# Kernel tuning notes

Hardware: AMD Instinct MI355X
Metric: run time of the kernel (lower is better)

## Reference

```python
import jax, jax.numpy as jnp
import numpy as np

M, K, N = 8192, 4096, 11008  # tokens, in_features, out_features


def setup_inputs() -> dict:
    key = jax.random.key(0)
    k_x, k_w, k_dq, k_is, k_qb = jax.random.split(key, 5)
    x = jax.random.normal(k_x, (M, K), dtype=jnp.float16)
    # int8 per-channel weights, values in [-127, 127]
    weight = jax.random.randint(k_w, (N, K), -127, 128, dtype=jnp.int32).astype(jnp.int8)
    # per-channel dequant scale ~ input_scale * weight_scale (small positive fp32)
    deq_scale = (jax.random.uniform(k_dq, (N,), dtype=jnp.float32) * 0.5 + 0.5) * 1e-4
    # per-tensor input scale (fp16 in the original buffer; kept fp32 here for math)
    input_scale = jax.random.uniform(k_is, (1,), dtype=jnp.float32) * 0.02 + 0.02
    quant_bias = jax.random.randint(k_qb, (N,), -100, 100, dtype=jnp.int32)
    input_offset = jnp.zeros((1,), dtype=jnp.int8)
    return {
        "x": x,
        "weight": weight,
        "deq_scale": deq_scale,
        "input_scale": input_scale,
        "quant_bias": quant_bias,
        "input_offset": input_offset,
    }


def reference(x, weight, deq_scale, input_scale, quant_bias, input_offset):
    # 1) static per-tensor activation quantization: fp16 -> int8
    inv_scale = 1.0 / input_scale.astype(jnp.float32)  # [1]
    xq = jnp.clip(
        jnp.round(x.astype(jnp.float32) * inv_scale) + input_offset.astype(jnp.float32),
        -128.0, 127.0,
    ).astype(jnp.int8)  # [M, K]
    acc = jnp.matmul(xq, weight.T, preferred_element_type=jnp.int32)  # [M, N] int32
    # 3) fused int32 bias add
    acc = acc + quant_bias[None, :]
    # 4) per-channel dequantization -> fp16 output
    out = (acc.astype(jnp.float32) * deq_scale[None, :]).astype(jnp.float16)
    return out
```

## Files before the change

kernel.cpp:

```cpp
#include <hip/hip_runtime.h>


#define MDIM 8192
#define KDIM 4096
#define NDIM 11008

#define BM 128
#define BN 128
#define BK 64
#define TM (MDIM / BM)
#define TN (NDIM / BN)
#define NWG (TM * TN)
#define CPX (NWG / 8)
#define KSTEPS (KDIM / BK)

using int32x4  = __attribute__((ext_vector_type(4))) int;
using int32x16 = __attribute__((ext_vector_type(16))) int;
using floatx4  = __attribute__((ext_vector_type(4))) float;
using uint32x2 = __attribute__((ext_vector_type(2))) unsigned int;

__device__ __forceinline__ void gload_lds16(const void* g, void* l) {
    __builtin_amdgcn_global_load_lds(
        (__attribute__((address_space(1))) unsigned int*)g,
        (__attribute__((address_space(3))) unsigned int*)l,
        16, 0, 0);
}

__device__ __forceinline__ int quant1(float f, float inv, float off) {
    float r = rintf(f * inv) + off;
    r = fminf(127.f, fmaxf(-128.f, r));
    return (int)r;
}

__device__ __forceinline__ int pack4i(int a, int b, int c, int d) {
    return (a & 255) | ((b & 255) << 8) | ((c & 255) << 16) | ((d & 255) << 24);
}

struct Resolved { const float* dq; const int* qb; };
__device__ __forceinline__ Resolved resolve4(const void* p11a, const void* p11b) {
    Resolved r;
    int a_is_dq = 1;
#pragma unroll
    for (int j = 0; j < 8; ++j) {
        const float v = ((const float*)p11a)[j];
        a_is_dq &= (v > 1e-6f) & (v < 1e-2f);
    }
    r.dq = a_is_dq ? (const float*)p11a : (const float*)p11b;
    r.qb = a_is_dq ? (const int*)p11b : (const int*)p11a;
    return r;
}

__device__ __forceinline__ void resolve_scale(const void* p1a, const void* p1b,
                                              float* inv, float* off) {
    const float fa = ((const float*)p1a)[0];
    const int a_is_isc = (fa > 1e-3f) & (fa < 1.0f);
    const float iscv = a_is_isc ? ((const float*)p1a)[0] : ((const float*)p1b)[0];
    *inv = 1.0f / iscv;
    *off = (float)(a_is_isc ? ((const int*)p1b)[0] : ((const int*)p1a)[0]);
}

__global__ __launch_bounds__(256)
void quant_x(const float* __restrict__ X, const void* p1a, const void* p1b,
             signed char* __restrict__ xq) {
    float inv, off;
    resolve_scale(p1a, p1b, &inv, &off);
    const long long nch = (long long)MDIM * KDIM / 8;
    const long long stride = (long long)gridDim.x * 256;
    for (long long i = (long long)blockIdx.x * 256 + threadIdx.x; i < nch; i += stride) {
        floatx4 v0 = ((const floatx4*)X)[2 * i];
        floatx4 v1 = ((const floatx4*)X)[2 * i + 1];
        int q[8];
#pragma unroll
        for (int j = 0; j < 4; ++j) {
            q[j]     = quant1(v0[j], inv, off);
            q[4 + j] = quant1(v1[j], inv, off);
        }
        uint32x2 o;
        o[0] = (unsigned)pack4i(q[0], q[1], q[2], q[3]);
        o[1] = (unsigned)pack4i(q[4], q[5], q[6], q[7]);
        ((uint32x2*)xq)[i] = o;
    }
}

__global__ __launch_bounds__(256)
void pack_w(const int* __restrict__ Wi, signed char* __restrict__ W8) {
    const long long nch = (long long)NDIM * KDIM / 8;
    const long long stride = (long long)gridDim.x * 256;
    for (long long i = (long long)blockIdx.x * 256 + threadIdx.x; i < nch; i += stride) {
        int32x4 a = ((const int32x4*)Wi)[2 * i];
        int32x4 b = ((const int32x4*)Wi)[2 * i + 1];
        uint32x2 o;
        o[0] = (unsigned)pack4i(a[0], a[1], a[2], a[3]);
        o[1] = (unsigned)pack4i(b[0], b[1], b[2], b[3]);
        ((uint32x2*)W8)[i] = o;
    }
}

__global__ __launch_bounds__(256, 3)
void gemm_i8(const signed char* __restrict__ Aq, const signed char* __restrict__ W8,
             const void* p11a, const void* p11b,
             float* __restrict__ out) {
    __shared__ alignas(16) signed char As[3][BM * BK];
    __shared__ alignas(16) signed char Bs[3][BN * BK];

    const int tid  = threadIdx.x;
    const int lane = tid & 63;
    const int wv   = tid >> 6;
    const int l5   = lane >> 5;
    const int lr   = lane & 31;
    const int wm   = wv >> 1;
    const int wn   = wv & 1;

    const int bid = blockIdx.x;
    const int wg  = (bid & 7) * CPX + (bid >> 3);
    int s, r;
    if (wg < 5120) { s = wg >> 9; r = wg & 511; }
    else           { s = 10;      r = wg - 5120; }
    const int w  = (s < 10) ? 8 : 6;
    const int gs = w << 3;
    const int g  = r / gs;
    const int t  = r % gs;
    const int m0 = ((g << 3) + t / w) * BM;
    const int n0 = (s * 8 + t % w) * BN;

    int32x16 acc[2][2];
#pragma unroll
    for (int i = 0; i < 2; ++i)
#pragma unroll
        for (int j = 0; j < 2; ++j)
#pragma unroll
            for (int e = 0; e < 16; ++e) acc[i][j][e] = 0;

    auto stage = [&](int buf, int kt) {
        const int kb = kt * BK;
#pragma unroll
        for (int j = 0; j < 2; ++j) {
            const int ci = (wv << 6) + (j << 8) + lane;
            const int rr = ci >> 2;
            const int pp = ci & 3;
            const int cc = pp ^ ((rr >> 1) & 3);
            gload_lds16(Aq + (size_t)(m0 + rr) * KDIM + kb + (cc << 4),
                        &As[buf][((wv << 6) + (j << 8)) << 4]);
            gload_lds16(W8 + (size_t)(n0 + rr) * KDIM + kb + (cc << 4),
                        &Bs[buf][((wv << 6) + (j << 8)) << 4]);
        }
    };

    stage(0, 0);
    stage(1, 1);

    int cur = 0, nb2 = 2;
    for (int kt = 0; kt < KSTEPS; ++kt) {
        if (kt + 2 < KSTEPS) {
            stage(nb2, kt + 2);
            asm volatile("s_waitcnt vmcnt(8)" ::: "memory");
        } else if (kt + 1 < KSTEPS) {
            asm volatile("s_waitcnt vmcnt(4)" ::: "memory");
        } else {
            asm volatile("s_waitcnt vmcnt(0)" ::: "memory");
        }
        __builtin_amdgcn_s_barrier();
        __builtin_amdgcn_sched_barrier(0);

        const signed char* Ab = As[cur];
        const signed char* Bb = Bs[cur];
        __builtin_amdgcn_s_setprio(1);
#pragma unroll
        for (int ks = 0; ks < 2; ++ks) {
            int32x4 af[2], bf[2];
#pragma unroll
            for (int mt = 0; mt < 2; ++mt) {
                const int rr = wm * 64 + mt * 32 + lr;
                const int pp = (ks * 2 + l5) ^ ((rr >> 1) & 3);
                af[mt] = *(const int32x4*)(Ab + (rr << 6) + (pp << 4));
            }
#pragma unroll
            for (int nt = 0; nt < 2; ++nt) {
                const int rr = wn * 64 + nt * 32 + lr;
                const int pp = (ks * 2 + l5) ^ ((rr >> 1) & 3);
                bf[nt] = *(const int32x4*)(Bb + (rr << 6) + (pp << 4));
            }
#pragma unroll
            for (int mt = 0; mt < 2; ++mt)
#pragma unroll
                for (int nt = 0; nt < 2; ++nt)
                    acc[mt][nt] = __builtin_amdgcn_mfma_i32_32x32x32_i8(
                        af[mt], bf[nt], acc[mt][nt], 0, 0, 0);
        }
        __builtin_amdgcn_s_setprio(0);
        __builtin_amdgcn_s_barrier();

        cur = (cur == 2) ? 0 : cur + 1;
        nb2 = (nb2 == 2) ? 0 : nb2 + 1;
    }

    const Resolved rs = resolve4(p11a, p11b);
#pragma unroll
    for (int nt = 0; nt < 2; ++nt) {
        const int gn   = n0 + wn * 64 + nt * 32 + lr;
        const int qbn  = rs.qb[gn];
        const float dq = rs.dq[gn];
#pragma unroll
        for (int mt = 0; mt < 2; ++mt) {
            const int gmb = m0 + wm * 64 + mt * 32 + (l5 << 2);
#pragma unroll
            for (int v = 0; v < 16; ++v) {
                const int gm = gmb + (v & 3) + ((v >> 2) << 3);
                out[(size_t)gm * NDIM + gn] = (float)(acc[mt][nt][v] + qbn) * dq;
            }
        }
    }
}

__global__ void codek(float* __restrict__ out) {
    out[blockIdx.x * 64 + threadIdx.x] = 51200.f;
}

extern "C" void kernel_launch(void* const* d_in, const int* in_sizes, int n_in,
                              void* d_out, int out_size, void* d_ws, size_t ws_size,
                              hipStream_t stream) {
    float* out = (float*)d_out;

    int ix = -1, iw = -1, i11[2] = {-1, -1}, i1[2] = {-1, -1};
    int n11 = 0, n1 = 0;
    bool bad = (n_in != 6);
    for (int i = 0; i < n_in && !bad; ++i) {
        const int s = in_sizes[i];
        if (s == MDIM * KDIM && ix < 0) ix = i;
        else if (s == NDIM * KDIM && iw < 0) iw = i;
        else if (s == NDIM && n11 < 2) i11[n11++] = i;
        else if (s == 1 && n1 < 2) i1[n1++] = i;
        else bad = true;
    }
    const size_t xq_bytes = (size_t)MDIM * KDIM;
    const size_t w8_bytes = (size_t)NDIM * KDIM;
    if (bad || ix < 0 || iw < 0 || n11 != 2 || n1 != 2 ||
        ws_size < xq_bytes + w8_bytes) {
        codek<<<dim3(100), dim3(64), 0, stream>>>(out);
        return;
    }

    const float* X  = (const float*)d_in[ix];
    const int*   Wi = (const int*)d_in[iw];
    const void*  pa = d_in[i11[0]];
    const void*  pb = d_in[i11[1]];
    const void*  pc = d_in[i1[0]];
    const void*  pd = d_in[i1[1]];

    signed char* xq = (signed char*)d_ws;
    signed char* w8 = xq + xq_bytes;

    quant_x<<<dim3(2048), dim3(256), 0, stream>>>(X, pc, pd, xq);
    pack_w<<<dim3(2048), dim3(256), 0, stream>>>(Wi, w8);
    gemm_i8<<<dim3(NWG), dim3(256), 0, stream>>>(xq, w8, pa, pb, out);
}
```

Baseline: 599.2 us.

## Replace direct global-to-LDS triple buffering with register-staged double buffering

The GEMM main loop no longer uses global_load_lds async copies into three LDS buffers. Each k-step now loads the next tile into registers, runs the MFMAs on the current buffer, and then writes the registers into the other of two LDS buffers before a single barrier. Global address offsets are also precomputed once. This cuts LDS use and may improve occupancy, but it adds VGPR pressure and an extra register-to-LDS write, and it shortens the prefetch distance from two steps to one.

```diff
diff --git a/kernel.cpp b/kernel.cpp
--- a/kernel.cpp
+++ b/kernel.cpp
@@ -18,13 +18,6 @@
 using int32x16 = __attribute__((ext_vector_type(16))) int;
 using floatx4  = __attribute__((ext_vector_type(4))) float;
 using uint32x2 = __attribute__((ext_vector_type(2))) unsigned int;
-
-__device__ __forceinline__ void gload_lds16(const void* g, void* l) {
-    __builtin_amdgcn_global_load_lds(
-        (__attribute__((address_space(1))) unsigned int*)g,
-        (__attribute__((address_space(3))) unsigned int*)l,
-        16, 0, 0);
-}
 
 __device__ __forceinline__ int quant1(float f, float inv, float off) {
     float r = rintf(f * inv) + off;
@@ -100,8 +93,8 @@
 void gemm_i8(const signed char* __restrict__ Aq, const signed char* __restrict__ W8,
              const void* p11a, const void* p11b,
              float* __restrict__ out) {
-    __shared__ alignas(16) signed char As[3][BM * BK];
-    __shared__ alignas(16) signed char Bs[3][BN * BK];
+    __shared__ alignas(16) signed char As[2][BM * BK];
+    __shared__ alignas(16) signed char Bs[2][BN * BK];
 
     const int tid  = threadIdx.x;
     const int lane = tid & 63;
@@ -131,35 +124,44 @@
 #pragma unroll
             for (int e = 0; e < 16; ++e) acc[i][j][e] = 0;
 
-    auto stage = [&](int buf, int kt) {
+    int lofs[2];
+    size_t gaofs[2], gbofs[2];
+#pragma unroll
+    for (int j = 0; j < 2; ++j) {
+        const int ci = (wv << 6) + (j << 8) + lane;
+        const int rr = ci >> 2;
+        const int pp = ci & 3;
+        const int cc = pp ^ ((rr >> 1) & 3);
+        lofs[j]  = ci << 4;
+        gaofs[j] = (size_t)(m0 + rr) * KDIM + (cc << 4);
+        gbofs[j] = (size_t)(n0 + rr) * KDIM + (cc << 4);
+    }
+
+    int32x4 pa[2], pb[2];
+    auto load = [&](int kt) {
         const int kb = kt * BK;
 #pragma unroll
         for (int j = 0; j < 2; ++j) {
-            const int ci = (wv << 6) + (j << 8) + lane;
-            const int rr = ci >> 2;
-            const int pp = ci & 3;
-            const int cc = pp ^ ((rr >> 1) & 3);
-            gload_lds16(Aq + (size_t)(m0 + rr) * KDIM + kb + (cc << 4),
-                        &As[buf][((wv << 6) + (j << 8)) << 4]);
-            gload_lds16(W8 + (size_t)(n0 + rr) * KDIM + kb + (cc << 4),
-                        &Bs[buf][((wv << 6) + (j << 8)) << 4]);
+            pa[j] = *(const int32x4*)(Aq + gaofs[j] + kb);
+            pb[j] = *(const int32x4*)(W8 + gbofs[j] + kb);
         }
     };
-
-    stage(0, 0);
-    stage(1, 1);
-
-    int cur = 0, nb2 = 2;
+    auto lwrite = [&](int buf) {
+#pragma unroll
+        for (int j = 0; j < 2; ++j) {
+            *(int32x4*)(&As[buf][lofs[j]]) = pa[j];
+            *(int32x4*)(&Bs[buf][lofs[j]]) = pb[j];
+        }
+    };
+
+    load(0);
+    lwrite(0);
+    asm volatile("s_waitcnt lgkmcnt(0)" ::: "memory");
+    __builtin_amdgcn_s_barrier();
+
     for (int kt = 0; kt < KSTEPS; ++kt) {
-        if (kt + 2 < KSTEPS) {
-            stage(nb2, kt + 2);
-            asm volatile("s_waitcnt vmcnt(8)" ::: "memory");
-        } else if (kt + 1 < KSTEPS) {
-            asm volatile("s_waitcnt vmcnt(4)" ::: "memory");
-        } else {
-            asm volatile("s_waitcnt vmcnt(0)" ::: "memory");
-        }
-        __builtin_amdgcn_s_barrier();
+        const int cur = kt & 1;
+        if (kt + 1 < KSTEPS) load(kt + 1);
         __builtin_amdgcn_sched_barrier(0);
 
         const signed char* Ab = As[cur];
@@ -188,10 +190,10 @@
                         af[mt], bf[nt], acc[mt][nt], 0, 0, 0);
         }
         __builtin_amdgcn_s_setprio(0);
+
+        if (kt + 1 < KSTEPS) lwrite(cur ^ 1);
+        asm volatile("s_waitcnt lgkmcnt(0)" ::: "memory");
         __builtin_amdgcn_s_barrier();
-
-        cur = (cur == 2) ? 0 : cur + 1;
-        nb2 = (nb2 == 2) ? 0 : nb2 + 1;
     }
 
     const Resolved rs = resolve4(p11a, p11b);
```

Result: no change. 594.0 us (-0.9%).

## Pre-tile and pre-swizzle quantized A and W into contiguous per-tile K-blocks

Applied to the files above, without the earlier changes.

The quantize and pack kernels now write int8 data in a tiled layout: each 128-row tile by 64-wide K block is stored contiguously, with the LDS XOR swizzle already applied. The GEMM staging loop then streams each tile's K blocks with linear, fully contiguous global_load_lds requests, replacing strided row reads. The intent is better DRAM/cache locality and simpler address arithmetic in the GEMM. In exchange, the prep kernels do less coalesced strided writes and use a different grid mapping, which may slow them down.

```diff
diff --git a/kernel.cpp b/kernel.cpp
--- a/kernel.cpp
+++ b/kernel.cpp
@@ -13,11 +13,11 @@
 #define NWG (TM * TN)
 #define CPX (NWG / 8)
 #define KSTEPS (KDIM / BK)
+#define TILEB (BM * BK)
 
 using int32x4  = __attribute__((ext_vector_type(4))) int;
 using int32x16 = __attribute__((ext_vector_type(16))) int;
 using floatx4  = __attribute__((ext_vector_type(4))) float;
-using uint32x2 = __attribute__((ext_vector_type(2))) unsigned int;
 
 __device__ __forceinline__ void gload_lds16(const void* g, void* l) {
     __builtin_amdgcn_global_load_lds(
@@ -60,48 +60,75 @@
 }
 
 __global__ __launch_bounds__(256)
-void quant_x(const float* __restrict__ X, const void* p1a, const void* p1b,
-             signed char* __restrict__ xq) {
+void quant_xT(const float* __restrict__ X, const void* p1a, const void* p1b,
+              signed char* __restrict__ xqT) {
     float inv, off;
     resolve_scale(p1a, p1b, &inv, &off);
-    const long long nch = (long long)MDIM * KDIM / 8;
-    const long long stride = (long long)gridDim.x * 256;
-    for (long long i = (long long)blockIdx.x * 256 + threadIdx.x; i < nch; i += stride) {
-        floatx4 v0 = ((const floatx4*)X)[2 * i];
-        floatx4 v1 = ((const floatx4*)X)[2 * i + 1];
-        int q[8];
-#pragma unroll
-        for (int j = 0; j < 4; ++j) {
-            q[j]     = quant1(v0[j], inv, off);
-            q[4 + j] = quant1(v1[j], inv, off);
-        }
-        uint32x2 o;
-        o[0] = (unsigned)pack4i(q[0], q[1], q[2], q[3]);
-        o[1] = (unsigned)pack4i(q[4], q[5], q[6], q[7]);
-        ((uint32x2*)xq)[i] = o;
+    const int mt   = blockIdx.x >> 4;
+    const int slab = blockIdx.x & 15;
+    const int t = threadIdx.x;
+    const int r = t & 127, h = t >> 7;
+    const float* src = X + (size_t)(mt * 128 + r) * KDIM;
+    signed char* db  = xqT + (size_t)mt * (KSTEPS * TILEB) + r * 64;
+    const int sw = (r >> 1) & 3;
+#pragma unroll
+    for (int it = 0; it < 2; ++it) {
+        const int kt = slab * 4 + h + 2 * it;
+        const float* s = src + kt * 64;
+        int pk[16];
+#pragma unroll
+        for (int i = 0; i < 16; ++i) {
+            floatx4 v = *(const floatx4*)(s + 4 * i);
+            pk[i] = pack4i(quant1(v[0], inv, off), quant1(v[1], inv, off),
+                           quant1(v[2], inv, off), quant1(v[3], inv, off));
+        }
+        signed char* d = db + (size_t)kt * TILEB;
+#pragma unroll
+        for (int c = 0; c < 4; ++c) {
+            int32x4 o;
+            o[0] = pk[c * 4]; o[1] = pk[c * 4 + 1];
+            o[2] = pk[c * 4 + 2]; o[3] = pk[c * 4 + 3];
+            *(int32x4*)(d + ((c ^ sw) << 4)) = o;
+        }
     }
 }
 
 __global__ __launch_bounds__(256)
-void pack_w(const int* __restrict__ Wi, signed char* __restrict__ W8) {
-    const long long nch = (long long)NDIM * KDIM / 8;
-    const long long stride = (long long)gridDim.x * 256;
-    for (long long i = (long long)blockIdx.x * 256 + threadIdx.x; i < nch; i += stride) {
-        int32x4 a = ((const int32x4*)Wi)[2 * i];
-        int32x4 b = ((const int32x4*)Wi)[2 * i + 1];
-        uint32x2 o;
-        o[0] = (unsigned)pack4i(a[0], a[1], a[2], a[3]);
-        o[1] = (unsigned)pack4i(b[0], b[1], b[2], b[3]);
-        ((uint32x2*)W8)[i] = o;
+void pack_wT(const int* __restrict__ Wi, signed char* __restrict__ w8T) {
+    const int nt   = blockIdx.x >> 4;
+    const int slab = blockIdx.x & 15;
+    const int t = threadIdx.x;
+    const int r = t & 127, h = t >> 7;
+    const int* src = Wi + (size_t)(nt * 128 + r) * KDIM;
+    signed char* db = w8T + (size_t)nt * (KSTEPS * TILEB) + r * 64;
+    const int sw = (r >> 1) & 3;
+#pragma unroll
+    for (int it = 0; it < 2; ++it) {
+        const int kt = slab * 4 + h + 2 * it;
+        const int* s = src + kt * 64;
+        int pk[16];
+#pragma unroll
+        for (int i = 0; i < 16; ++i) {
+            int32x4 v = *(const int32x4*)(s + 4 * i);
+            pk[i] = pack4i(v[0], v[1], v[2], v[3]);
+        }
+        signed char* d = db + (size_t)kt * TILEB;
+#pragma unroll
+        for (int c = 0; c < 4; ++c) {
+            int32x4 o;
+            o[0] = pk[c * 4]; o[1] = pk[c * 4 + 1];
+            o[2] = pk[c * 4 + 2]; o[3] = pk[c * 4 + 3];
+            *(int32x4*)(d + ((c ^ sw) << 4)) = o;
+        }
     }
 }
 
 __global__ __launch_bounds__(256, 3)
-void gemm_i8(const signed char* __restrict__ Aq, const signed char* __restrict__ W8,
+void gemm_i8(const signed char* __restrict__ AqT, const signed char* __restrict__ W8T,
              const void* p11a, const void* p11b,
              float* __restrict__ out) {
-    __shared__ alignas(16) signed char As[3][BM * BK];
-    __shared__ alignas(16) signed char Bs[3][BN * BK];
+    __shared__ alignas(16) signed char As[3][TILEB];
+    __shared__ alignas(16) signed char Bs[3][TILEB];
 
     const int tid  = threadIdx.x;
     const int lane = tid & 63;
@@ -120,8 +147,13 @@
     const int gs = w << 3;
     const int g  = r / gs;
     const int t  = r % gs;
-    const int m0 = ((g << 3) + t / w) * BM;
-    const int n0 = (s * 8 + t % w) * BN;
+    const int mtile = (g << 3) + t / w;
+    const int ntile = s * 8 + t % w;
+    const int m0 = mtile * BM;
+    const int n0 = ntile * BN;
+
+    const signed char* Abase = AqT + (size_t)mtile * (KSTEPS * TILEB);
+    const signed char* Bbase = W8T + (size_t)ntile * (KSTEPS * TILEB);
 
     int32x16 acc[2][2];
 #pragma unroll
@@ -132,17 +164,12 @@
             for (int e = 0; e < 16; ++e) acc[i][j][e] = 0;
 
     auto stage = [&](int buf, int kt) {
-        const int kb = kt * BK;
+        const size_t ka = (size_t)kt * TILEB;
 #pragma unroll
         for (int j = 0; j < 2; ++j) {
-            const int ci = (wv << 6) + (j << 8) + lane;
-            const int rr = ci >> 2;
-            const int pp = ci & 3;
-            const int cc = pp ^ ((rr >> 1) & 3);
-            gload_lds16(Aq + (size_t)(m0 + rr) * KDIM + kb + (cc << 4),
-                        &As[buf][((wv << 6) + (j << 8)) << 4]);
-            gload_lds16(W8 + (size_t)(n0 + rr) * KDIM + kb + (cc << 4),
-                        &Bs[buf][((wv << 6) + (j << 8)) << 4]);
+            const int co = (wv << 6) + (j << 8);
+            gload_lds16(Abase + ka + ((co + lane) << 4), &As[buf][co << 4]);
+            gload_lds16(Bbase + ka + ((co + lane) << 4), &Bs[buf][co << 4]);
         }
     };
 
@@ -247,10 +274,10 @@
     const void*  pc = d_in[i1[0]];
     const void*  pd = d_in[i1[1]];
 
-    signed char* xq = (signed char*)d_ws;
-    signed char* w8 = xq + xq_bytes;
-
-    quant_x<<<dim3(2048), dim3(256), 0, stream>>>(X, pc, pd, xq);
-    pack_w<<<dim3(2048), dim3(256), 0, stream>>>(Wi, w8);
-    gemm_i8<<<dim3(NWG), dim3(256), 0, stream>>>(xq, w8, pa, pb, out);
-}
+    signed char* xqT = (signed char*)d_ws;
+    signed char* w8T = xqT + xq_bytes;
+
+    quant_xT<<<dim3(TM * 16), dim3(256), 0, stream>>>(X, pc, pd, xqT);
+    pack_wT<<<dim3(TN * 16), dim3(256), 0, stream>>>(Wi, w8T);
+    gemm_i8<<<dim3(NWG), dim3(256), 0, stream>>>(xqT, w8T, pa, pb, out);
+}
```

New measurement: 588.1 us. No clear change (-1.9%).
